# Performance work log

Hardware: AMD Instinct MI355X
Metric: run time of the kernel (lower is better)

The kernel has to match this reference:

```python
import jax, jax.numpy as jnp
import numpy as np

GROUPS = 1024
K_N = 32
FEAT_DIM = 64
EPS = 1e-05


def farthest_point_sample(xyz, npoint):
    # xyz: [B, N, 3] -> centroids [B, npoint] int32
    # Original torch code starts from a random point; we use index 0 for determinism.
    B, N, _ = xyz.shape

    def step(carry, _):
        distance, farthest = carry
        centroid = jnp.take_along_axis(xyz, farthest[:, None, None], axis=1)  # [B,1,3]
        dist = jnp.sum((xyz - centroid) ** 2, axis=-1)  # [B,N]
        distance = jnp.minimum(distance, dist)
        new_far = jnp.argmax(distance, axis=-1).astype(jnp.int32)
        return (distance, new_far), farthest

    init = (jnp.full((B, N), 1e10, dtype=xyz.dtype), jnp.zeros((B,), jnp.int32))
    _, cents = jax.lax.scan(step, init, None, length=npoint)
    return cents.T  # [B, npoint]


def index_points(points, idx):
    # points: [B, N, C]; idx: [B, ...] -> [B, ..., C]
    B = points.shape[0]
    bidx = jnp.arange(B).reshape((B,) + (1,) * (idx.ndim - 1))
    return points[bidx, idx]


def square_distance(src, dst):
    # src [B,S,C], dst [B,N,C] -> [B,S,N]
    d = -2.0 * jnp.einsum('bsc,bnc->bsn', src, dst)
    d = d + jnp.sum(src ** 2, -1)[:, :, None]
    d = d + jnp.sum(dst ** 2, -1)[:, None, :]
    return d


def setup_inputs() -> dict:
    key = jax.random.key(0)
    k1, k2 = jax.random.split(key)
    xyz = jax.random.normal(k1, (8, 3, 4096), dtype=jnp.float32)
    feats = jax.random.normal(k2, (8, FEAT_DIM, 4096), dtype=jnp.float32)
    affine_alpha_p = jnp.ones((1, 1, 1, FEAT_DIM), jnp.float32)
    affine_beta_p = jnp.zeros((1, 1, 1, FEAT_DIM), jnp.float32)
    return {"xyz": xyz, "feats": feats,
            "affine_alpha_p": affine_alpha_p, "affine_beta_p": affine_beta_p}


def reference(xyz, feats, affine_alpha_p, affine_beta_p):
    xyz = jnp.transpose(xyz, (0, 2, 1))      # [B,N,3]
    feats = jnp.transpose(feats, (0, 2, 1))  # [B,N,D]
    B, N, _ = xyz.shape
    S, k = GROUPS, K_N

    fps_idx = farthest_point_sample(xyz, S)          # [B,S]
    new_xyz = index_points(xyz, fps_idx)             # [B,S,3]
    new_feats = index_points(feats, fps_idx)         # [B,S,D]

    sqr = square_distance(new_xyz, xyz)              # [B,S,N]
    _, idx = jax.lax.top_k(-sqr, k)                  # smallest-k -> [B,S,k]
    grouped = index_points(feats, idx)               # [B,S,k,D]

    mean = new_feats[:, :, None, :]                  # [B,S,1,D]
    diff = grouped - mean
    # torch.std over flattened per-batch, unbiased (ddof=1)
    std = jnp.std(diff.reshape(B, -1), axis=-1, ddof=1)[:, None, None, None]
    grouped = diff / (std + EPS)
    grouped = affine_alpha_p * grouped + affine_beta_p

    point_feats = jnp.concatenate(
        [grouped, grouped - new_feats[:, :, None, :]], axis=-1)  # [B,S,k,2D]

    new_feats_out = jnp.transpose(new_feats, (0, 2, 1))          # [B,D,S]
    new_xyz_out = jnp.transpose(new_xyz, (0, 2, 1))              # [B,3,S]
    point_feats_out = jnp.transpose(point_feats, (0, 3, 1, 2))   # [B,2D,S,k]
    return (new_xyz_out, new_feats_out, point_feats_out)
```

## Files before the change

kernel.cpp:

```cpp
#include <hip/hip_runtime.h>

#define NPTS 4096
#define NSAMP 1024
#define KNN_K 32
#define FDIM 64
#define EPSF 1e-5f

#define DPP_MAX64(CTRL)                                                          \
  {                                                                              \
    unsigned _olo = (unsigned)__builtin_amdgcn_update_dpp(0, (int)klo, CTRL,     \
                                                          0xf, 0xf, true);       \
    unsigned _ohi = (unsigned)__builtin_amdgcn_update_dpp(0, (int)khi, CTRL,     \
                                                          0xf, 0xf, true);       \
    unsigned long long _ok = ((unsigned long long)_ohi << 32) | _olo;            \
    unsigned long long _ck = ((unsigned long long)khi << 32) | klo;              \
    if (_ok > _ck) { klo = _olo; khi = _ohi; }                                   \
  }

__global__ __launch_bounds__(512) void fps_kernel(const float* __restrict__ xyz,
                                                  int* __restrict__ fps_idx,
                                                  float* __restrict__ sqnorm) {
  __shared__ float4 pts[NPTS];
  __shared__ unsigned long long skeys[2][8];
  const int b = blockIdx.x, t = threadIdx.x;
  const int lane = t & 63, w = t >> 6;
  const float* xb = xyz + (size_t)b * 3 * NPTS;
  float px[8], py[8], pz[8], dist[8];
#pragma unroll
  for (int k = 0; k < 8; ++k) {
    int p = k * 512 + t;
    float x = xb[p], y = xb[NPTS + p], z = xb[2 * NPTS + p];
    float sq = __fadd_rn(__fadd_rn(__fmul_rn(x, x), __fmul_rn(y, y)),
                         __fmul_rn(z, z));
    px[k] = x; py[k] = y; pz[k] = z; dist[k] = 1e10f;
    pts[p] = make_float4(x, y, z, sq);
    sqnorm[b * NPTS + p] = sq;
  }
  if (t == 0) fps_idx[b * NSAMP] = 0;
  __syncthreads();
  int far = 0;
  for (int it = 1; it < NSAMP; ++it) {
    float4 c = pts[far];
    float bv = -1.0f;
    int bi = 0;
#pragma unroll
    for (int k = 0; k < 8; ++k) {
      float dx = __fsub_rn(px[k], c.x);
      float dy = __fsub_rn(py[k], c.y);
      float dz = __fsub_rn(pz[k], c.z);
      float dd = __fadd_rn(__fadd_rn(__fmul_rn(dx, dx), __fmul_rn(dy, dy)),
                           __fmul_rn(dz, dz));
      float nd = fminf(dist[k], dd);
      dist[k] = nd;
      if (nd > bv) { bv = nd; bi = k * 512 + t; }
    }
    unsigned bvb = __float_as_uint(bv);
    unsigned klo = (bvb << 12) | (unsigned)(4095 - bi);
    unsigned khi = bvb >> 20;
    DPP_MAX64(0x111)
    DPP_MAX64(0x112)
    DPP_MAX64(0x114)
    DPP_MAX64(0x118)
    DPP_MAX64(0x142)
    DPP_MAX64(0x143)
    if (lane == 63) skeys[it & 1][w] = ((unsigned long long)khi << 32) | klo;
    __syncthreads();
    unsigned long long kk = skeys[it & 1][lane & 7];
    klo = (unsigned)kk;
    khi = (unsigned)(kk >> 32);
    DPP_MAX64(0x111)
    DPP_MAX64(0x112)
    DPP_MAX64(0x114)
    unsigned flo = (unsigned)__builtin_amdgcn_readlane((int)klo, 7);
    far = 4095 - (int)(flo & 0xfffu);
    if (t == 0) fps_idx[b * NSAMP + it] = far;
  }
}

__global__ __launch_bounds__(256) void gather_feats_kernel(const float* __restrict__ feats,
                                                           const int* __restrict__ fps,
                                                           float* __restrict__ out1,
                                                           float* __restrict__ nf) {
  int i = blockIdx.x * 256 + threadIdx.x;
  int s = i & 1023, c = (i >> 10) & 63, b = i >> 16;
  int p = fps[(b << 10) + s];
  float v = feats[((size_t)(b * 64 + c)) * NPTS + p];
  out1[(b * 64 + c) * 1024 + s] = v;
  nf[(((b << 10) + s) << 6) + c] = v;
}

__global__ __launch_bounds__(256) void gather_xyz_kernel(const float* __restrict__ xyz,
                                                         const float* __restrict__ sqnorm,
                                                         const int* __restrict__ fps,
                                                         float* __restrict__ out0,
                                                         float4* __restrict__ nx4) {
  int i = blockIdx.x * 256 + threadIdx.x;
  int b = i >> 10, s = i & 1023;
  int p = fps[i];
  const float* xb = xyz + (size_t)b * 3 * NPTS;
  float x = xb[p], y = xb[NPTS + p], z = xb[2 * NPTS + p];
  nx4[i] = make_float4(x, y, z, sqnorm[b * NPTS + p]);
  out0[(b * 3 + 0) * 1024 + s] = x;
  out0[(b * 3 + 1) * 1024 + s] = y;
  out0[(b * 3 + 2) * 1024 + s] = z;
}

__device__ __forceinline__ unsigned long long mk_key(float xn, float yn, float zn,
                                                     float sq, float cx, float cy,
                                                     float cz, float src2, int n) {
  float dot = __fmaf_rn(zn, cz, __fmaf_rn(yn, cy, __fmul_rn(xn, cx)));
  float d = __fadd_rn(__fadd_rn(__fmul_rn(-2.0f, dot), src2), sq);
  unsigned mb = __float_as_uint(d);
  mb = (mb & 0x80000000u) ? ~mb : (mb | 0x80000000u);
  return ((unsigned long long)mb << 32) | (unsigned)n;
}

__global__ __launch_bounds__(256, 2) void knn_kernel(const float* __restrict__ xyz,
                                                     const float* __restrict__ sqnorm,
                                                     const float4* __restrict__ nx4,
                                                     int* __restrict__ knn) {
  const int lane = threadIdx.x & 63;
  const int w = threadIdx.x >> 6;
  const int row = blockIdx.x * 4 + w;
  const int b = row >> 10;
  const float4 c4 = nx4[row];
  const float cx = c4.x, cy = c4.y, cz = c4.z, src2 = c4.w;
  const float4* x4 = (const float4*)(xyz + (size_t)b * 3 * NPTS);
  const float4* y4 = (const float4*)(xyz + (size_t)b * 3 * NPTS + NPTS);
  const float4* z4 = (const float4*)(xyz + (size_t)b * 3 * NPTS + 2 * NPTS);
  const float4* s4 = (const float4*)(sqnorm + (size_t)b * NPTS);
  unsigned long long key[64];
#pragma unroll
  for (int jj = 0; jj < 16; ++jj) {
    int vi = jj * 64 + lane;
    float4 xv = x4[vi], yv = y4[vi], zv = z4[vi], sv = s4[vi];
    int n0 = vi * 4;
    key[jj * 4 + 0] = mk_key(xv.x, yv.x, zv.x, sv.x, cx, cy, cz, src2, n0);
    key[jj * 4 + 1] = mk_key(xv.y, yv.y, zv.y, sv.y, cx, cy, cz, src2, n0 + 1);
    key[jj * 4 + 2] = mk_key(xv.z, yv.z, zv.z, sv.z, cx, cy, cz, src2, n0 + 2);
    key[jj * 4 + 3] = mk_key(xv.w, yv.w, zv.w, sv.w, cx, cy, cz, src2, n0 + 3);
  }
  unsigned long long last = 0ull;
  const int out_base = row * KNN_K;
#pragma unroll 1
  for (int r = 0; r < KNN_K; ++r) {
    unsigned long long cur = ~0ull;
#pragma unroll
    for (int j = 0; j < 64; ++j) {
      unsigned long long k = key[j];
      if (k > last && k < cur) cur = k;
    }
#pragma unroll
    for (int off = 32; off > 0; off >>= 1) {
      unsigned long long o = __shfl_xor(cur, off);
      cur = (o < cur) ? o : cur;
    }
    last = cur;
    if (lane == r) knn[out_base + r] = (int)(unsigned)(cur & 0xffffffffull);
  }
}

__global__ __launch_bounds__(256) void stats_kernel(const float* __restrict__ feats,
                                                    const float* __restrict__ nf,
                                                    const int* __restrict__ knn,
                                                    double* __restrict__ stats) {
  const int b = blockIdx.x >> 5;
  const int chunk = blockIdx.x & 31;
  const int base = chunk * 65536;
  double sm = 0.0, sq = 0.0;
  for (int i = 0; i < 256; ++i) {
    int e = base + i * 256 + threadIdx.x;
    int c = e >> 15;
    int sk = e & 32767;
    int s = sk >> 5, j = sk & 31;
    int p = knn[((((b << 10) + s)) << 5) + j];
    float f = feats[((size_t)(b * 64 + c)) * NPTS + p];
    float m = nf[(((b << 10) + s) << 6) + c];
    double d = (double)__fsub_rn(f, m);
    sm += d;
    sq += d * d;
  }
#pragma unroll
  for (int off = 32; off > 0; off >>= 1) {
    sm += __shfl_down(sm, off);
    sq += __shfl_down(sq, off);
  }
  __shared__ double red[8];
  int w = threadIdx.x >> 6;
  if ((threadIdx.x & 63) == 0) { red[w * 2] = sm; red[w * 2 + 1] = sq; }
  __syncthreads();
  if (threadIdx.x == 0) {
    atomicAdd(&stats[b * 2 + 0], red[0] + red[2] + red[4] + red[6]);
    atomicAdd(&stats[b * 2 + 1], red[1] + red[3] + red[5] + red[7]);
  }
}

__global__ __launch_bounds__(256) void out_kernel(const float* __restrict__ feats,
                                                  const float* __restrict__ nf,
                                                  const int* __restrict__ knn,
                                                  const double* __restrict__ stats,
                                                  const float* __restrict__ alpha,
                                                  const float* __restrict__ beta,
                                                  float* __restrict__ out2) {
  const int plane = blockIdx.x;
  const int b = plane >> 6, c = plane & 63;
  const int sk = blockIdx.y * 256 + threadIdx.x;
  const int s = sk >> 5, j = sk & 31;
  const double n = 2097152.0;
  double sm = stats[b * 2], sqs = stats[b * 2 + 1];
  double var = (sqs - sm * sm / n) / (n - 1.0);
  float stdf = (float)sqrt(var);
  float denom = stdf + EPSF;
  int p = knn[((((b << 10) + s)) << 5) + j];
  float f = feats[((size_t)(b * 64 + c)) * NPTS + p];
  float m = nf[(((b << 10) + s) << 6) + c];
  float diff = __fsub_rn(f, m);
  float g = alpha[c] * (diff / denom) + beta[c];
  size_t o1 = (((size_t)(b * 128 + c) << 10) + (size_t)s) * 32 + j;
  size_t o2 = (((size_t)(b * 128 + 64 + c) << 10) + (size_t)s) * 32 + j;
  out2[o1] = g;
  out2[o2] = g - m;
}

extern "C" void kernel_launch(void* const* d_in, const int* in_sizes, int n_in,
                              void* d_out, int out_size, void* d_ws, size_t ws_size,
                              hipStream_t stream) {
  (void)in_sizes; (void)n_in; (void)out_size; (void)ws_size;
  const float* xyz   = (const float*)d_in[0];
  const float* feats = (const float*)d_in[1];
  const float* alpha = (const float*)d_in[2];
  const float* beta  = (const float*)d_in[3];
  float* out  = (float*)d_out;
  float* out0 = out;
  float* out1 = out + 24576;
  float* out2 = out + 24576 + 524288;

  char* ws = (char*)d_ws;
  int*    fps   = (int*)ws;
  float*  sqn   = (float*)(ws + 32768);
  float4* nx4   = (float4*)(ws + 163840);
  float*  nf    = (float*)(ws + 294912);
  int*    knn   = (int*)(ws + 2392064);
  double* stats = (double*)(ws + 3440640);

  hipMemsetAsync(stats, 0, 128, stream);
  fps_kernel<<<8, 512, 0, stream>>>(xyz, fps, sqn);
  gather_feats_kernel<<<2048, 256, 0, stream>>>(feats, fps, out1, nf);
  gather_xyz_kernel<<<32, 256, 0, stream>>>(xyz, sqn, fps, out0, nx4);
  knn_kernel<<<2048, 256, 0, stream>>>(xyz, sqn, nx4, knn);
  stats_kernel<<<256, 256, 0, stream>>>(feats, nf, knn, stats);
  out_kernel<<<dim3(512, 128), 256, 0, stream>>>(feats, nf, knn, stats, alpha, beta, out2);
}
```

Measured before the change: 950.2 us.

## Shrink FPS block to 4 waves with 16 points per thread and tree max

The farthest-point-sampling kernel now runs with 256 threads, each holding 16 points instead of 8. This cuts the cross-wave reduction to 4 waves and shortens the barrier cost in each of the 1023 serial iterations. The per-thread argmax becomes a balanced fmax tree followed by a select pass over precomputed reversed indices. Sample indices are buffered in shared memory and written to global memory once at the end. The trade-off is more serial ALU work per thread and higher register pressure, in exchange for cheaper synchronisation per iteration.

```diff
diff --git a/kernel.cpp b/kernel.cpp
--- a/kernel.cpp
+++ b/kernel.cpp
@@ -17,45 +17,53 @@
     if (_ok > _ck) { klo = _olo; khi = _ohi; }                                   \
   }
 
-__global__ __launch_bounds__(512) void fps_kernel(const float* __restrict__ xyz,
+__global__ __launch_bounds__(256) void fps_kernel(const float* __restrict__ xyz,
                                                   int* __restrict__ fps_idx,
                                                   float* __restrict__ sqnorm) {
   __shared__ float4 pts[NPTS];
-  __shared__ unsigned long long skeys[2][8];
+  __shared__ unsigned long long skeys[2][4];
+  __shared__ int fpsb[NSAMP];
   const int b = blockIdx.x, t = threadIdx.x;
   const int lane = t & 63, w = t >> 6;
   const float* xb = xyz + (size_t)b * 3 * NPTS;
-  float px[8], py[8], pz[8], dist[8];
-#pragma unroll
-  for (int k = 0; k < 8; ++k) {
-    int p = k * 512 + t;
+  float px[16], py[16], pz[16], dist[16];
+  unsigned rik[16];
+#pragma unroll
+  for (int k = 0; k < 16; ++k) {
+    int p = k * 256 + t;
     float x = xb[p], y = xb[NPTS + p], z = xb[2 * NPTS + p];
     float sq = __fadd_rn(__fadd_rn(__fmul_rn(x, x), __fmul_rn(y, y)),
                          __fmul_rn(z, z));
     px[k] = x; py[k] = y; pz[k] = z; dist[k] = 1e10f;
+    rik[k] = 4095u - (unsigned)p;
     pts[p] = make_float4(x, y, z, sq);
     sqnorm[b * NPTS + p] = sq;
   }
-  if (t == 0) fps_idx[b * NSAMP] = 0;
+  if (t == 0) fpsb[0] = 0;
   __syncthreads();
-  int far = 0;
+  float4 c = pts[0];
   for (int it = 1; it < NSAMP; ++it) {
-    float4 c = pts[far];
-    float bv = -1.0f;
-    int bi = 0;
-#pragma unroll
-    for (int k = 0; k < 8; ++k) {
+#pragma unroll
+    for (int k = 0; k < 16; ++k) {
       float dx = __fsub_rn(px[k], c.x);
       float dy = __fsub_rn(py[k], c.y);
       float dz = __fsub_rn(pz[k], c.z);
       float dd = __fadd_rn(__fadd_rn(__fmul_rn(dx, dx), __fmul_rn(dy, dy)),
                            __fmul_rn(dz, dz));
-      float nd = fminf(dist[k], dd);
-      dist[k] = nd;
-      if (nd > bv) { bv = nd; bi = k * 512 + t; }
+      dist[k] = fminf(dist[k], dd);
     }
-    unsigned bvb = __float_as_uint(bv);
-    unsigned klo = (bvb << 12) | (unsigned)(4095 - bi);
+    float m01 = fmaxf(dist[0], dist[1]),  m23 = fmaxf(dist[2], dist[3]);
+    float m45 = fmaxf(dist[4], dist[5]),  m67 = fmaxf(dist[6], dist[7]);
+    float m89 = fmaxf(dist[8], dist[9]),  mab = fmaxf(dist[10], dist[11]);
+    float mcd = fmaxf(dist[12], dist[13]), mef = fmaxf(dist[14], dist[15]);
+    float q0 = fmaxf(m01, m23), q1 = fmaxf(m45, m67);
+    float q2 = fmaxf(m89, mab), q3 = fmaxf(mcd, mef);
+    float mv = fmaxf(fmaxf(q0, q1), fmaxf(q2, q3));
+    unsigned ri = rik[15];
+#pragma unroll
+    for (int k = 15; k >= 0; --k) ri = (dist[k] == mv) ? rik[k] : ri;
+    unsigned bvb = __float_as_uint(mv);
+    unsigned klo = (bvb << 12) | ri;
     unsigned khi = bvb >> 20;
     DPP_MAX64(0x111)
     DPP_MAX64(0x112)
@@ -65,16 +73,20 @@
     DPP_MAX64(0x143)
     if (lane == 63) skeys[it & 1][w] = ((unsigned long long)khi << 32) | klo;
     __syncthreads();
-    unsigned long long kk = skeys[it & 1][lane & 7];
+    unsigned long long kk = skeys[it & 1][lane & 3];
     klo = (unsigned)kk;
     khi = (unsigned)(kk >> 32);
     DPP_MAX64(0x111)
     DPP_MAX64(0x112)
-    DPP_MAX64(0x114)
-    unsigned flo = (unsigned)__builtin_amdgcn_readlane((int)klo, 7);
-    far = 4095 - (int)(flo & 0xfffu);
-    if (t == 0) fps_idx[b * NSAMP + it] = far;
-  }
+    unsigned flo = (unsigned)__builtin_amdgcn_readlane((int)klo, 3);
+    int far = 4095 - (int)(flo & 0xfffu);
+    if (t == 0) fpsb[it] = far;
+    c = pts[far];
+  }
+  __syncthreads();
+#pragma unroll
+  for (int k = 0; k < 4; ++k)
+    fps_idx[b * NSAMP + k * 256 + t] = fpsb[k * 256 + t];
 }
 
 __global__ __launch_bounds__(256) void gather_feats_kernel(const float* __restrict__ feats,
@@ -244,7 +256,7 @@
   double* stats = (double*)(ws + 3440640);
 
   hipMemsetAsync(stats, 0, 128, stream);
-  fps_kernel<<<8, 512, 0, stream>>>(xyz, fps, sqn);
+  fps_kernel<<<8, 256, 0, stream>>>(xyz, fps, sqn);
   gather_feats_kernel<<<2048, 256, 0, stream>>>(feats, fps, out1, nf);
   gather_xyz_kernel<<<32, 256, 0, stream>>>(xyz, sqn, fps, out0, nx4);
   knn_kernel<<<2048, 256, 0, stream>>>(xyz, sqn, nx4, knn);
```

Measured after the change: 969.6 us. 2.1% more time.
